# Optimization experiments

Hardware: AMD Instinct MI355X
Metric: run time of the kernel (lower is better)

## Reference

```python
import jax, jax.numpy as jnp
import numpy as np
from jax import lax
from jax.scipy.linalg import solve_triangular

# Newton-Schulz dynamic coefficients (6 iterations), from the source table
NS_COEFFS = [
    (3955/1024, -8306/1024, 5008/1024),
    (3735/1024, -6681/1024, 3463/1024),
    (3799/1024, -6499/1024, 3211/1024),
    (4019/1024, -6385/1024, 2906/1024),
    (2677/1024, -3029/1024, 1162/1024),
    (2172/1024, -1833/1024,  682/1024),
]

B, T, D, H, DK, DV = 4, 1024, 512, 8, 64, 64


def newton_schulz6(M):
    # M: (..., dv, dk), square (dv == dk) so no transpose branch is needed
    X = M / (jnp.linalg.norm(M, axis=(-2, -1), keepdims=True) + 1e-7)
    for a, b, c in NS_COEFFS:
        A = X @ jnp.swapaxes(X, -1, -2)
        Bm = b * A + c * (A @ A)
        X = a * X + Bm @ X
    return X


def setup_inputs() -> dict:
    key = jax.random.key(0)
    ks = jax.random.split(key, 9)
    s = 0.02  # weight init scale
    return {
        "x":  jax.random.normal(ks[0], (B, T, D), jnp.float32),
        "Wq": jax.random.normal(ks[1], (H * DK, D), jnp.float32) * s,
        "Wk": jax.random.normal(ks[2], (H * DK, D), jnp.float32) * s,
        "Wv": jax.random.normal(ks[3], (H * DV, D), jnp.float32) * s,
        "Ww": jax.random.normal(ks[4], (H * DK, D), jnp.float32) * s,
        "Wp": jax.random.normal(ks[5], (H * 2, D), jnp.float32) * s,
        "Wo": jax.random.normal(ks[6], (D, H * DV), jnp.float32) * s,
        "S0": jax.random.normal(ks[7], (H, DV, DK), jnp.float32),
        "M0": jnp.zeros((H, DV, DK), jnp.float32),
    }


def _forward(x, Wq, Wk, Wv, Ww, Wp, Wo, S0, M0):
    b, t, d = x.shape
    h, dv, dk = S0.shape

    def heads(W, e):  # (b,t,d) @ W.T -> (b,h,t,e)
        return (x @ W.T).reshape(b, t, h, e).transpose(0, 2, 1, 3)

    q = heads(Wq, dk)
    k = heads(Wk, dk)
    v = heads(Wv, dv)
    w = heads(Ww, dk)
    p = jax.nn.sigmoid((x @ Wp.T).reshape(b, t, h, 2).transpose(0, 2, 1, 3))
    eta, theta = p[..., 0], p[..., 1]  # (b,h,t)

    # delta-rule redundancy: u_t = v_t - softmax(w_t K_{<t}^T / sqrt(dk)) U_{<t}
    scores = jnp.einsum('bhtd,bhsd->bhts', w, k) / (dk ** 0.5)
    strict = jnp.tril(jnp.ones((t, t), bool), k=-1)  # s < t
    A = jax.nn.softmax(jnp.where(strict, scores, -1e30), axis=-1) * strict
    # (I + A) U = V  (unit lower-triangular solve == the sequential recurrence)
    U = solve_triangular(A, v, lower=True, unit_diagonal=True)  # (b,h,t,dv)

    # sequential state update over time (momentum + Newton-Schulz + S accumulation)
    tm = lambda a: jnp.moveaxis(a, 2, 0)  # time-major
    xs = (tm(U), tm(k), tm(q), jnp.moveaxis(eta, 2, 0), jnp.moveaxis(theta, 2, 0))

    @jax.checkpoint
    def step(carry, inp):
        S, M = carry
        u_t, k_t, q_t, eta_t, theta_t = inp  # (b,h,dv)/(b,h,dk)/(b,h)
        g = u_t[..., :, None] * k_t[..., None, :]        # (b,h,dv,dk)
        th = theta_t[..., None, None]
        M = th * M + (1.0 - th) * g
        Sp = newton_schulz6(M)
        S = S + eta_t[..., None, None] * Sp
        o = jnp.einsum('bhvk,bhk->bhv', S, q_t)
        return (S, M), o

    S_init = jnp.broadcast_to(S0, (b, h, dv, dk))
    M_init = jnp.broadcast_to(M0, (b, h, dv, dk))
    (_, _), O = lax.scan(step, (S_init, M_init), xs)  # O: (t,b,h,dv)

    o = O.transpose(1, 0, 2, 3).reshape(b, t, h * dv)
    return o @ Wo.T  # (b,t,d)


def reference(x, Wq, Wk, Wv, Ww, Wp, Wo, S0, M0):
    return _forward(x, Wq, Wk, Wv, Ww, Wp, Wo, S0, M0)
```

## Files before the change

### kernel.cpp

```cpp
#include <hip/hip_runtime.h>
#include <hip/hip_bf16.h>
#include <math.h>

#define Bn 4
#define Tn 1024
#define Dn 512
#define Hn 8
#define BHn 32
#define LDP 65
#define LDU 68
#define LH 72

typedef _Float16 f16x8 __attribute__((ext_vector_type(8)));
typedef _Float16 f16x4 __attribute__((ext_vector_type(4)));
typedef float    f32x4 __attribute__((ext_vector_type(4)));

__constant__ float NS_Ac[6] = {3955.0f/1024.0f, 3735.0f/1024.0f, 3799.0f/1024.0f,
                               4019.0f/1024.0f, 2677.0f/1024.0f, 2172.0f/1024.0f};
__constant__ float NS_Bc[6] = {-8306.0f/1024.0f, -6681.0f/1024.0f, -6499.0f/1024.0f,
                               -6385.0f/1024.0f, -3029.0f/1024.0f, -1833.0f/1024.0f};
__constant__ float NS_Cc[6] = {5008.0f/1024.0f, 3463.0f/1024.0f, 3211.0f/1024.0f,
                               2906.0f/1024.0f, 1162.0f/1024.0f,  682.0f/1024.0f};

__device__ __forceinline__ f32x4 mfma16(f16x4 a, f16x4 b, f32x4 c) {
  return __builtin_amdgcn_mfma_f32_16x16x16f16(a, b, c, 0, 0, 0);
}
__device__ __forceinline__ f32x4 mfma32(f16x8 a, f16x8 b, f32x4 c) {
  return __builtin_amdgcn_mfma_f32_16x16x32_f16(a, b, c, 0, 0, 0);
}

__device__ __forceinline__ f16x4 cvt4(f32x4 a) {
  f16x4 h;
  h[0] = (_Float16)a[0]; h[1] = (_Float16)a[1];
  h[2] = (_Float16)a[2]; h[3] = (_Float16)a[3];
  return h;
}

__device__ __forceinline__ f16x4 cvt4rtz(f32x4 a) {
  const auto lo = __builtin_amdgcn_cvt_pkrtz(a[0], a[1]);
  const auto hi = __builtin_amdgcn_cvt_pkrtz(a[2], a[3]);
  f16x4 h;
  h[0] = (_Float16)lo[0]; h[1] = (_Float16)lo[1];
  h[2] = (_Float16)hi[0]; h[3] = (_Float16)hi[1];
  return h;
}

__device__ __forceinline__ f16x8 pack8(f16x4 lo, f16x4 hi) {
  f16x8 o;
  o[0] = lo[0]; o[1] = lo[1]; o[2] = lo[2]; o[3] = lo[3];
  o[4] = hi[0]; o[5] = hi[1]; o[6] = hi[2]; o[7] = hi[3];
  return o;
}

__device__ __forceinline__ void set_half(f16x8& v, int h, f16x4 x) {
  if (h) { v[4] = x[0]; v[5] = x[1]; v[6] = x[2]; v[7] = x[3]; }
  else   { v[0] = x[0]; v[1] = x[1]; v[2] = x[2]; v[3] = x[3]; }
}

__device__ __forceinline__ f16x4 make_If(int r, int g) {
  const int dd = r - 4 * g;
  f16x4 If;
  If[0] = (dd == 0) ? (_Float16)1.f : (_Float16)0.f;
  If[1] = (dd == 1) ? (_Float16)1.f : (_Float16)0.f;
  If[2] = (dd == 2) ? (_Float16)1.f : (_Float16)0.f;
  If[3] = (dd == 3) ? (_Float16)1.f : (_Float16)0.f;
  return If;
}

__device__ __forceinline__ f16x8 ld_frag8(const _Float16* lds, int row, int c, int g) {
  const f16x4 lo = *reinterpret_cast<const f16x4*>(lds + row * LH + (2 * c) * 16 + 4 * g);
  const f16x4 hi = *reinterpret_cast<const f16x4*>(lds + row * LH + (2 * c + 1) * 16 + 4 * g);
  return pack8(lo, hi);
}



__device__ __forceinline__ void stage_tile_h(_Float16* __restrict__ dst,
                                             const float* __restrict__ src,
                                             int srcStride, int tid) {
#pragma unroll
  for (int i = 0; i < 4; ++i) {
    const int idx = tid + (i << 8);
    const int row = idx >> 4;
    const int c4  = (idx & 15) << 2;
    const float4 v = *reinterpret_cast<const float4*>(src + (size_t)row * srcStride + c4);
    f16x4 h;
    h[0] = (_Float16)v.x; h[1] = (_Float16)v.y; h[2] = (_Float16)v.z; h[3] = (_Float16)v.w;
    *reinterpret_cast<f16x4*>(dst + row * LH + c4) = h;
  }
}

__device__ __forceinline__ void stage_tile_u(float* __restrict__ dst,
                                             const float* __restrict__ src, int tid) {
#pragma unroll
  for (int i = 0; i < 4; ++i) {
    const int idx = tid + (i << 8);
    const int row = idx >> 4;
    const int c4  = (idx & 15) << 2;
    *reinterpret_cast<float4*>(dst + row * LDU + c4) =
        *reinterpret_cast<const float4*>(src + (size_t)row * 64 + c4);
  }
}

__device__ __forceinline__ void tri_solve_blocked(const float* __restrict__ Sc,
                                                  float* __restrict__ Ua, int tid) {
  const int dv = tid & 63;
  const int grp = tid >> 6;
#pragma unroll 1
  for (int db = 0; db < 4; ++db) {
    const int base = db * 16;
    if (grp == 0) {
#pragma unroll 1
      for (int rr = 1; rr < 16; ++rr) {
        float s = 0.f;
        for (int c = 0; c < rr; ++c)
          s = fmaf(Sc[(base + rr) * LDP + base + c], Ua[(base + c) * LDU + dv], s);
        Ua[(base + rr) * LDU + dv] -= s;
      }
    }
    __syncthreads();
    if (db < 3) {
      for (int r2 = base + 16 + grp; r2 < 64; r2 += 4) {
        float s = 0.f;
#pragma unroll
        for (int c = 0; c < 16; ++c)
          s = fmaf(Sc[r2 * LDP + base + c], Ua[(base + c) * LDU + dv], s);
        Ua[r2 * LDU + dv] -= s;
      }
    }
    __syncthreads();
  }
}


__global__ __launch_bounds__(256) void proj4_kernel(
    const float* __restrict__ x,
    const float* __restrict__ W0, const float* __restrict__ W1,
    const float* __restrict__ W2, const float* __restrict__ W3,
    float* __restrict__ o0, float* __restrict__ o1,
    float* __restrict__ o2, float* __restrict__ o3) {
  __shared__ __align__(16) _Float16 Af[64 * LH];
  __shared__ __align__(16) _Float16 Bf[64 * LH];
  const float* W; float* outp;
  switch (blockIdx.z) {
    case 0:  W = W0; outp = o0; break;
    case 1:  W = W1; outp = o1; break;
    case 2:  W = W2; outp = o2; break;
    default: W = W3; outp = o3; break;
  }
  const int tid = threadIdx.x;
  const int m0 = blockIdx.x * 64;
  const int n0 = blockIdx.y * 64;
  const int wid = tid >> 6, lane = tid & 63;
  const int r = lane & 15, g = lane >> 4;
  f32x4 acc[4] = {};
  for (int kt = 0; kt < Dn; kt += 64) {
    stage_tile_h(Af, x + (size_t)m0 * Dn + kt, Dn, tid);
    stage_tile_h(Bf, W + (size_t)n0 * Dn + kt, Dn, tid);
    __syncthreads();
    f16x8 a8[2];
#pragma unroll
    for (int c = 0; c < 2; ++c) a8[c] = ld_frag8(Af, 16 * wid + r, c, g);
#pragma unroll
    for (int jb = 0; jb < 4; ++jb) {
#pragma unroll
      for (int c = 0; c < 2; ++c)
        acc[jb] = mfma32(a8[c], ld_frag8(Bf, 16 * jb + r, c, g), acc[jb]);
    }
    __syncthreads();
  }
#pragma unroll
  for (int jb = 0; jb < 4; ++jb)
#pragma unroll
    for (int d = 0; d < 4; ++d) {
      const int m = m0 + 16 * wid + 4 * g + d;
      const int n = n0 + 16 * jb + r;
      const int b = m >> 10, t = m & 1023, h = n >> 6, e = n & 63;
      outp[(((size_t)(b * Hn + h)) * Tn + t) * 64 + e] = acc[jb][d];
    }
}

#define XSTR 516
__global__ __launch_bounds__(256) void wp_kernel(const float* __restrict__ x,
                                                 const float* __restrict__ Wp,
                                                 float* __restrict__ eta,
                                                 float* __restrict__ theta) {
  __shared__ float xs[16 * XSTR];
  __shared__ float wps[16 * XSTR];
  const int tid = threadIdx.x;
  const int r0 = blockIdx.x * 16;
#pragma unroll
  for (int i = 0; i < 8; ++i) {
    const int idx = tid + (i << 8);
    const int r = idx >> 7, c4 = (idx & 127) << 2;
    const float4 v = *reinterpret_cast<const float4*>(x + (size_t)(r0 + r) * Dn + c4);
    float* p = xs + r * XSTR + c4;
    p[0] = v.x; p[1] = v.y; p[2] = v.z; p[3] = v.w;
    const float4 wv = *reinterpret_cast<const float4*>(Wp + (size_t)r * Dn + c4);
    float* pw = wps + r * XSTR + c4;
    pw[0] = wv.x; pw[1] = wv.y; pw[2] = wv.z; pw[3] = wv.w;
  }
  __syncthreads();
  const int row = tid >> 4, col = tid & 15;
  float acc = 0.f;
#pragma unroll 8
  for (int k = 0; k < Dn; ++k) acc = fmaf(xs[row * XSTR + k], wps[col * XSTR + k], acc);
  const float sg = 1.f / (1.f + __expf(-acc));
  const int m = r0 + row, b = m >> 10, t = m & 1023, h = col >> 1;
  float* dst = (col & 1) ? theta : eta;
  dst[((size_t)(b * Hn + h)) * Tn + t] = sg;
}

__global__ __launch_bounds__(256) void rowstats_kernel(
    const float* __restrict__ wb, const float* __restrict__ kb,
    float* __restrict__ rowm, float* __restrict__ rowl) {
  __shared__ __align__(16) _Float16 Wh[64 * LH];
  __shared__ __align__(16) _Float16 Kh[64 * LH];
  const int tb = blockIdx.x, bh = blockIdx.y, t0 = tb * 64;
  const int tid = threadIdx.x, wid = tid >> 6, lane = tid & 63;
  const int r = lane & 15, g = lane >> 4;
  stage_tile_h(Wh, wb + ((size_t)bh * Tn + t0) * 64, 64, tid);
  float rm[4], rl[4];
#pragma unroll
  for (int d = 0; d < 4; ++d) { rm[d] = -INFINITY; rl[d] = 0.f; }
  __syncthreads();
  f16x8 wfr8[2];
#pragma unroll
  for (int c = 0; c < 2; ++c) wfr8[c] = ld_frag8(Wh, 16 * wid + r, c, g);
  for (int sb = 0; sb <= tb; ++sb) {
    __syncthreads();
    stage_tile_h(Kh, kb + ((size_t)bh * Tn + sb * 64) * 64, 64, tid);
    __syncthreads();
    float sv[4][4];
    float tmax[4] = {-INFINITY, -INFINITY, -INFINITY, -INFINITY};
#pragma unroll
    for (int jb = 0; jb < 4; ++jb) {
      f32x4 acc = {0.f, 0.f, 0.f, 0.f};
#pragma unroll
      for (int c = 0; c < 2; ++c)
        acc = mfma32(wfr8[c], ld_frag8(Kh, 16 * jb + r, c, g), acc);
      const int col = sb * 64 + 16 * jb + r;
#pragma unroll
      for (int d = 0; d < 4; ++d) {
        const int row = t0 + 16 * wid + 4 * g + d;
        const float s = (col < row) ? acc[d] * 0.125f : -INFINITY;
        sv[jb][d] = s;
        tmax[d] = fmaxf(tmax[d], s);
      }
    }
#pragma unroll
    for (int m = 1; m < 16; m <<= 1)
#pragma unroll
      for (int d = 0; d < 4; ++d) tmax[d] = fmaxf(tmax[d], __shfl_xor(tmax[d], m, 64));
#pragma unroll
    for (int d = 0; d < 4; ++d) {
      const float mnew  = fmaxf(rm[d], tmax[d]);
      const float msafe = (mnew == -INFINITY) ? 0.f : mnew;
      float s = __expf(sv[0][d] - msafe) + __expf(sv[1][d] - msafe) +
                __expf(sv[2][d] - msafe) + __expf(sv[3][d] - msafe);
#pragma unroll
      for (int m = 1; m < 16; m <<= 1) s += __shfl_xor(s, m, 64);
      const float scale = (rm[d] == -INFINITY) ? 0.f : __expf(rm[d] - msafe);
      rl[d] = rl[d] * scale + s;
      rm[d] = mnew;
    }
  }
  if (r == 0) {
#pragma unroll
    for (int d = 0; d < 4; ++d) {
      const int row = t0 + 16 * wid + 4 * g + d;
      rowm[(size_t)bh * Tn + row] = rm[d];
      rowl[(size_t)bh * Tn + row] = (rl[d] == 0.f) ? 1.f : rl[d];
    }
  }
}

__global__ __launch_bounds__(256) void copyU_kernel(const float* __restrict__ vb,
                                                    float* __restrict__ Ub) {
  const int gid = blockIdx.x * 256 + threadIdx.x;
  ((float4*)Ub)[gid] = ((const float4*)vb)[gid];
}

__global__ __launch_bounds__(256) void solve_diag0_kernel(
    const float* __restrict__ wb, const float* __restrict__ kb,
    const float* __restrict__ vb, const float* __restrict__ rowm,
    const float* __restrict__ rowl, float* __restrict__ Ub) {
  __shared__ __align__(16) _Float16 Wh[64 * LH];
  __shared__ __align__(16) _Float16 Kh[64 * LH];
  __shared__ float Sc[64 * LDP];
  __shared__ __align__(16) float Ua[64 * LDU];
  __shared__ float rmL[64], rlL[64];
  const int bh = blockIdx.x;
  const int tid = threadIdx.x, wid = tid >> 6, lane = tid & 63;
  const int r = lane & 15, g = lane >> 4;
  stage_tile_h(Wh, wb + (size_t)bh * Tn * 64, 64, tid);
  stage_tile_h(Kh, kb + (size_t)bh * Tn * 64, 64, tid);
  stage_tile_u(Ua, vb + (size_t)bh * Tn * 64, tid);
  if (tid < 64) { rmL[tid] = rowm[(size_t)bh * Tn + tid]; rlL[tid] = rowl[(size_t)bh * Tn + tid]; }
  __syncthreads();
  f16x4 wfr[4];
#pragma unroll
  for (int kc = 0; kc < 4; ++kc)
    wfr[kc] = *reinterpret_cast<const f16x4*>(Wh + (16 * wid + r) * LH + kc * 16 + 4 * g);
  float rmv[4], rlv[4];
#pragma unroll
  for (int d = 0; d < 4; ++d) {
    rmv[d] = rmL[16 * wid + 4 * g + d];
    rlv[d] = rlL[16 * wid + 4 * g + d];
  }
#pragma unroll
  for (int jb = 0; jb < 4; ++jb) {
    f32x4 acc = {0.f, 0.f, 0.f, 0.f};
#pragma unroll
    for (int kc = 0; kc < 4; ++kc)
      acc = mfma16(wfr[kc],
                   *reinterpret_cast<const f16x4*>(Kh + (16 * jb + r) * LH + kc * 16 + 4 * g),
                   acc);
#pragma unroll
    for (int d = 0; d < 4; ++d) {
      const int lr = 16 * wid + 4 * g + d, lc = 16 * jb + r;
      Sc[lr * LDP + lc] = (lc < lr) ? __expf(acc[d] * 0.125f - rmv[d]) / rlv[d] : 0.f;
    }
  }
  __syncthreads();
  tri_solve_blocked(Sc, Ua, tid);
#pragma unroll
  for (int i = 0; i < 4; ++i) {
    const int idx = tid + (i << 8);
    const int row = idx >> 4, c4 = (idx & 15) << 2;
    *reinterpret_cast<float4*>(Ub + ((size_t)bh * Tn + row) * 64 + c4) =
        *reinterpret_cast<const float4*>(Ua + row * LDU + c4);
  }
}

__global__ __launch_bounds__(256) void solve_step_kernel(
    const float* __restrict__ wb, const float* __restrict__ kb,
    const float* __restrict__ rowm, const float* __restrict__ rowl,
    float* __restrict__ Ub, int ib) {
  __shared__ __align__(16) _Float16 Wh[64 * LH];
  __shared__ __align__(16) _Float16 Kh[64 * LH];
  __shared__ __align__(16) _Float16 UTh[64 * LH];
  __shared__ float Sc[64 * LDP];
  __shared__ __align__(16) float Ua[64 * LDU];
  __shared__ float rmL[64], rlL[64];
  const int f = ib + 1 + blockIdx.x, bh = blockIdx.y;
  const int tid = threadIdx.x, wid = tid >> 6, lane = tid & 63;
  const int r = lane & 15, g = lane >> 4;
  stage_tile_h(Wh, wb + ((size_t)bh * Tn + f * 64) * 64, 64, tid);
  stage_tile_h(Kh, kb + ((size_t)bh * Tn + ib * 64) * 64, 64, tid);
  {
    const float* src = Ub + ((size_t)bh * Tn + ib * 64) * 64;
#pragma unroll
    for (int i2 = 0; i2 < 4; ++i2) {
      const int idx = tid + (i2 << 8);
      const int row = idx >> 4, c4 = (idx & 15) << 2;
      const float4 v = *reinterpret_cast<const float4*>(src + (size_t)row * 64 + c4);
      UTh[(c4 + 0) * LH + row] = (_Float16)v.x;
      UTh[(c4 + 1) * LH + row] = (_Float16)v.y;
      UTh[(c4 + 2) * LH + row] = (_Float16)v.z;
      UTh[(c4 + 3) * LH + row] = (_Float16)v.w;
    }
  }
  if (tid < 64) {
    rmL[tid] = rowm[(size_t)bh * Tn + f * 64 + tid];
    rlL[tid] = rowl[(size_t)bh * Tn + f * 64 + tid];
  }
  __syncthreads();
  f16x4 wfr[4];
#pragma unroll
  for (int kc = 0; kc < 4; ++kc)
    wfr[kc] = *reinterpret_cast<const f16x4*>(Wh + (16 * wid + r) * LH + kc * 16 + 4 * g);
  float rmv[4], rlv[4];
#pragma unroll
  for (int d = 0; d < 4; ++d) {
    rmv[d] = rmL[16 * wid + 4 * g + d];
    rlv[d] = rlL[16 * wid + 4 * g + d];
  }
  const f16x4 If = make_If(r, g);
  f16x4 Pfr[4];
#pragma unroll
  for (int jb = 0; jb < 4; ++jb) {
    f32x4 acc = {0.f, 0.f, 0.f, 0.f};
#pragma unroll
    for (int kc = 0; kc < 4; ++kc)
      acc = mfma16(wfr[kc],
                   *reinterpret_cast<const f16x4*>(Kh + (16 * jb + r) * LH + kc * 16 + 4 * g),
                   acc);
    f16x4 pf;
#pragma unroll
    for (int d = 0; d < 4; ++d)
      pf[d] = (_Float16)(-__expf(acc[d] * 0.125f - rmv[d]) / rlv[d]);
    Pfr[jb] = cvt4(mfma16(pf, If, (f32x4){0.f, 0.f, 0.f, 0.f}));
  }
  const float* uf = Ub + ((size_t)bh * Tn + f * 64) * 64;
  f32x4 acc2[4];
#pragma unroll
  for (int i = 0; i < 4; ++i) {
    const float4 v = *reinterpret_cast<const float4*>(uf + (size_t)(16 * wid + r) * 64 + 16 * i + 4 * g);
    acc2[i][0] = v.x; acc2[i][1] = v.y; acc2[i][2] = v.z; acc2[i][3] = v.w;
#pragma unroll
    for (int kc = 0; kc < 4; ++kc)
      acc2[i] = mfma16(*reinterpret_cast<const f16x4*>(UTh + (16 * i + r) * LH + kc * 16 + 4 * g),
                       Pfr[kc], acc2[i]);
  }
  if (f == ib + 1) {
    __syncthreads();
    stage_tile_h(Kh, kb + ((size_t)bh * Tn + f * 64) * 64, 64, tid);
#pragma unroll
    for (int i = 0; i < 4; ++i) {
      float4 v = {acc2[i][0], acc2[i][1], acc2[i][2], acc2[i][3]};
      *reinterpret_cast<float4*>(Ua + (16 * wid + r) * LDU + 16 * i + 4 * g) = v;
    }
    __syncthreads();
#pragma unroll
    for (int jb = 0; jb < 4; ++jb) {
      f32x4 acc = {0.f, 0.f, 0.f, 0.f};
#pragma unroll
      for (int kc = 0; kc < 4; ++kc)
        acc = mfma16(wfr[kc],
                     *reinterpret_cast<const f16x4*>(Kh + (16 * jb + r) * LH + kc * 16 + 4 * g),
                     acc);
#pragma unroll
      for (int d = 0; d < 4; ++d) {
        const int lr = 16 * wid + 4 * g + d, lc = 16 * jb + r;
        Sc[lr * LDP + lc] = (lc < lr) ? __expf(acc[d] * 0.125f - rmv[d]) / rlv[d] : 0.f;
      }
    }
    __syncthreads();
    tri_solve_blocked(Sc, Ua, tid);
#pragma unroll
    for (int i2 = 0; i2 < 4; ++i2) {
      const int idx = tid + (i2 << 8);
      const int row = idx >> 4, c4 = (idx & 15) << 2;
      *reinterpret_cast<float4*>(Ub + ((size_t)bh * Tn + f * 64 + row) * 64 + c4) =
          *reinterpret_cast<const float4*>(Ua + row * LDU + c4);
    }
  } else {
#pragma unroll
    for (int i = 0; i < 4; ++i) {
      float4 v = {acc2[i][0], acc2[i][1], acc2[i][2], acc2[i][3]};
      *reinterpret_cast<float4*>(Ub + ((size_t)bh * Tn + f * 64 + 16 * wid + r) * 64 + 16 * i + 4 * g) = v;
    }
  }
}

__global__ __launch_bounds__(256) void mscan_kernel(
    const float* __restrict__ Ub, const float* __restrict__ kb,
    const float* __restrict__ theta, float* __restrict__ Mcarry,
    _Float16* __restrict__ Mbuf, int t0, int Tc) {
  const int gid = blockIdx.x * 256 + threadIdx.x;
  const int bh = gid >> 12, p = gid & 4095;
  const int q = p >> 9, i = q >> 1, c = q & 1;
  const int l = (p >> 3) & 63, g = l >> 4, r = l & 15;
  const int s = p & 7, jhi = s >> 2, jlo = s & 3;
  const int dv = i * 16 + r;
  const int dk = c * 32 + jhi * 16 + g * 4 + jlo;
  float M = Mcarry[gid];
  const float* Urow = Ub + (size_t)bh * Tn * 64;
  const float* krow = kb + (size_t)bh * Tn * 64;
  const float* th   = theta + (size_t)bh * Tn;
  for (int tl = 0; tl < Tc; ++tl) {
    const int t = t0 + tl;
    const float thv = th[t];
    const float gg = Urow[(size_t)t * 64 + dv] * krow[(size_t)t * 64 + dk];
    M = thv * M + (1.f - thv) * gg;
    Mbuf[((size_t)bh * Tc + tl) * 4096 + p] = (_Float16)M;
  }
  Mcarry[gid] = M;
}

__global__ __launch_bounds__(256, 4) void ns_kernel(_Float16* __restrict__ Mbuf) {
  const int tid  = threadIdx.x;
  const int wid  = tid >> 6, lane = tid & 63;
  const int r    = lane & 15, g = lane >> 4;
  _Float16* src = Mbuf + ((size_t)blockIdx.x * 4 + wid) * 4096;

  f16x8 Xf8[4][2];
  float ss = 0.f;
#pragma unroll
  for (int i = 0; i < 4; ++i)
#pragma unroll
    for (int c = 0; c < 2; ++c) {
      const f16x8 h = *reinterpret_cast<const f16x8*>(src + (i * 2 + c) * 512 + lane * 8);
#pragma unroll
      for (int d = 0; d < 8; ++d) { const float f = (float)h[d]; ss += f * f; }
      Xf8[i][c] = h;
    }
#pragma unroll
  for (int off = 32; off > 0; off >>= 1) ss += __shfl_xor(ss, off, 64);
  const float inv = 1.f / (sqrtf(ss) + 1e-7f);
#pragma unroll
  for (int i = 0; i < 4; ++i)
#pragma unroll
    for (int c = 0; c < 2; ++c) {
      f32x4 lo, hi;
#pragma unroll
      for (int d = 0; d < 4; ++d) { lo[d] = (float)Xf8[i][c][d] * inv; hi[d] = (float)Xf8[i][c][d + 4] * inv; }
      Xf8[i][c] = pack8(cvt4rtz(lo), cvt4rtz(hi));
    }

  const f16x4 If = make_If(r, g);
  f16x4 zero4;
  zero4[0] = (_Float16)0.f; zero4[1] = (_Float16)0.f;
  zero4[2] = (_Float16)0.f; zero4[3] = (_Float16)0.f;
  const f16x8 I8[2] = {pack8(If, zero4), pack8(zero4, If)};
  float Iw[4];
  Iw[0] = (float)If[0]; Iw[1] = (float)If[1]; Iw[2] = (float)If[2]; Iw[3] = (float)If[3];

  f16x8 Ff8[4][2];
  f32x4 acc[4][4];

#pragma unroll 1
  for (int it = 0; it < 6; ++it) {
    const float ca = NS_Ac[it], cb = NS_Bc[it], cc = NS_Cc[it];
#pragma unroll
    for (int i = 0; i < 4; ++i)
#pragma unroll
      for (int j = i; j < 4; ++j) {
        f32x4 a = mfma32(Xf8[i][0], Xf8[j][0], (f32x4){0.f, 0.f, 0.f, 0.f});
        acc[i][j] = mfma32(Xf8[i][1], Xf8[j][1], a);
      }
#pragma unroll
    for (int i = 0; i < 4; ++i) {
      {
        const f16x4 t = cvt4rtz(mfma32(Xf8[i][i >> 1], I8[i & 1], (f32x4){0.f, 0.f, 0.f, 0.f}));
        set_half(Xf8[i][i >> 1], i & 1, t);
      }
#pragma unroll
      for (int j = i + 1; j < 4; ++j) {
        const f16x4 t1 = cvt4rtz(mfma32(Xf8[i][j >> 1], I8[j & 1], (f32x4){0.f, 0.f, 0.f, 0.f}));
        const f16x4 t2 = cvt4rtz(mfma32(Xf8[j][i >> 1], I8[i & 1], (f32x4){0.f, 0.f, 0.f, 0.f}));
        set_half(Xf8[j][i >> 1], i & 1, t1);
        set_half(Xf8[i][j >> 1], j & 1, t2);
      }
    }
#pragma unroll
    for (int i = 0; i < 4; ++i)
#pragma unroll
      for (int j = i; j < 4; ++j) set_half(Ff8[j][i >> 1], i & 1, cvt4rtz(acc[i][j]));
#pragma unroll
    for (int i = 0; i < 4; ++i)
#pragma unroll
      for (int j = i + 1; j < 4; ++j)
        set_half(Ff8[i][j >> 1], j & 1,
                 cvt4rtz(mfma32(Ff8[j][i >> 1], I8[i & 1], (f32x4){0.f, 0.f, 0.f, 0.f})));
    const float bc = cb / cc;
#pragma unroll
    for (int i = 0; i < 4; ++i)
#pragma unroll
      for (int j = i; j < 4; ++j) {
        f32x4 a = acc[i][j];
        a[0] *= bc; a[1] *= bc; a[2] *= bc; a[3] *= bc;
        a = mfma32(Ff8[i][0], Ff8[j][0], a);
        a = mfma32(Ff8[i][1], Ff8[j][1], a);
        a[0] *= cc; a[1] *= cc; a[2] *= cc; a[3] *= cc;
        acc[i][j] = a;
      }
#pragma unroll
    for (int i = 0; i < 4; ++i)
#pragma unroll
      for (int d = 0; d < 4; ++d) acc[i][i][d] = fmaf(ca, Iw[d], acc[i][i][d]);
#pragma unroll
    for (int i = 0; i < 4; ++i)
#pragma unroll
      for (int j = i; j < 4; ++j) set_half(Ff8[j][i >> 1], i & 1, cvt4rtz(acc[i][j]));
#pragma unroll
    for (int i = 0; i < 4; ++i)
#pragma unroll
      for (int j = i + 1; j < 4; ++j)
        set_half(Ff8[i][j >> 1], j & 1,
                 cvt4rtz(mfma32(Ff8[j][i >> 1], I8[i & 1], (f32x4){0.f, 0.f, 0.f, 0.f})));
#pragma unroll
    for (int i = 0; i < 4; ++i)
#pragma unroll
      for (int j = 0; j < 4; ++j) {
        f32x4 a = mfma32(Xf8[i][0], Ff8[j][0], (f32x4){0.f, 0.f, 0.f, 0.f});
        acc[i][j] = mfma32(Xf8[i][1], Ff8[j][1], a);
      }
    const bool last = (it == 5);
#pragma unroll
    for (int i = 0; i < 4; ++i)
#pragma unroll
      for (int j = 0; j < 4; ++j)
        set_half(Xf8[j][i >> 1], i & 1, last ? cvt4(acc[i][j]) : cvt4rtz(acc[i][j]));
  }

#pragma unroll
  for (int i = 0; i < 4; ++i)
#pragma unroll
    for (int c = 0; c < 2; ++c)
      *reinterpret_cast<f16x8*>(src + (i * 2 + c) * 512 + lane * 8) = Xf8[i][c];
}

__global__ __launch_bounds__(256) void gsum_kernel(
    const float* __restrict__ eta, const _Float16* __restrict__ Mbuf,
    float* __restrict__ Gbuf, int t0, int Tc) {
  const int j = blockIdx.x, bh = blockIdx.y, tid = threadIdx.x;
  const int nsub = Tc >> 4;
  float acc[16] = {};
#pragma unroll 1
  for (int i = 0; i < 16; ++i) {
    const int tl = j * 16 + i;
    const float ev = eta[(size_t)bh * Tn + t0 + tl];
    const _Float16* sp = Mbuf + ((size_t)bh * Tc + tl) * 4096;
    const f16x8 h0 = *reinterpret_cast<const f16x8*>(sp + tid * 8);
    const f16x8 h1 = *reinterpret_cast<const f16x8*>(sp + 2048 + tid * 8);
#pragma unroll
    for (int u = 0; u < 8; ++u) {
      acc[u]     += ev * (float)h0[u];
      acc[8 + u] += ev * (float)h1[u];
    }
  }
  float* g = Gbuf + ((size_t)bh * nsub + j) * 4096;
#pragma unroll
  for (int u = 0; u < 2; ++u) {
    float4 w0 = {acc[u*4], acc[u*4+1], acc[u*4+2], acc[u*4+3]};
    *reinterpret_cast<float4*>(g + tid * 8 + u * 4) = w0;
    float4 w1 = {acc[8+u*4], acc[8+u*4+1], acc[8+u*4+2], acc[8+u*4+3]};
    *reinterpret_cast<float4*>(g + 2048 + tid * 8 + u * 4) = w1;
  }
}

__global__ __launch_bounds__(256) void sbase_kernel(
    float* __restrict__ Scarry, const float* __restrict__ Gbuf,
    float* __restrict__ Sbase, int Tc) {
  const int gid = blockIdx.x * 256 + threadIdx.x;
  const int bh = gid >> 12, e = gid & 4095;
  const int nsub = Tc >> 4;
  float S = Scarry[gid];
  for (int j = 0; j < nsub; ++j) {
    const size_t idx = ((size_t)bh * nsub + j) * 4096 + e;
    Sbase[idx] = S;
    S += Gbuf[idx];
  }
  Scarry[gid] = S;
}

__global__ __launch_bounds__(256) void outv2_kernel(
    const float* __restrict__ eta, const float* __restrict__ qb,
    const float* __restrict__ Sbase, const _Float16* __restrict__ Mbuf,
    float* __restrict__ ob, int t0, int Tc) {
  const int j = blockIdx.x, bh = blockIdx.y, tid = threadIdx.x;
  const int nsub = Tc >> 4;
  const int ty = tid >> 4, tx = tid & 15;
  const int dv0 = ty * 4, dk0 = tx * 4;
  int off[4];
#pragma unroll
  for (int r2 = 0; r2 < 4; ++r2) {
    const int row = dv0 + r2;
    off[r2] = ((row >> 4) * 2 + (dk0 >> 5)) * 512 +
              (((dk0 & 15) >> 2) * 16 + (row & 15)) * 8 + ((dk0 >> 4) & 1) * 4;
  }
  float S[4][4];
  const float* sb = Sbase + ((size_t)bh * nsub + j) * 4096;
#pragma unroll
  for (int r2 = 0; r2 < 4; ++r2) {
    const float4 v = *reinterpret_cast<const float4*>(sb + off[r2]);
    S[r2][0] = v.x; S[r2][1] = v.y; S[r2][2] = v.z; S[r2][3] = v.w;
  }
#pragma unroll 1
  for (int i = 0; i < 16; ++i) {
    const int tl = j * 16 + i, t = t0 + tl;
    const float ev = eta[(size_t)bh * Tn + t];
    const float4 q4 = *reinterpret_cast<const float4*>(qb + ((size_t)bh * Tn + t) * 64 + dk0);
    const _Float16* sp = Mbuf + ((size_t)bh * Tc + tl) * 4096;
    float part[4];
#pragma unroll
    for (int r2 = 0; r2 < 4; ++r2) {
      const f16x4 h = *reinterpret_cast<const f16x4*>(sp + off[r2]);
      S[r2][0] += ev * (float)h[0];
      S[r2][1] += ev * (float)h[1];
      S[r2][2] += ev * (float)h[2];
      S[r2][3] += ev * (float)h[3];
      part[r2] = S[r2][0] * q4.x + S[r2][1] * q4.y + S[r2][2] * q4.z + S[r2][3] * q4.w;
    }
#pragma unroll
    for (int m = 1; m < 16; m <<= 1)
#pragma unroll
      for (int r2 = 0; r2 < 4; ++r2) part[r2] += __shfl_xor(part[r2], m, 64);
    if (tx == 0) {
      float4 o4 = {part[0], part[1], part[2], part[3]};
      *reinterpret_cast<float4*>(ob + ((size_t)bh * Tn + t) * 64 + dv0) = o4;
    }
  }
}

__global__ __launch_bounds__(256) void init_carry_kernel(
    const float* __restrict__ S0, const float* __restrict__ M0,
    float* __restrict__ Scarry, float* __restrict__ Mcarry) {
  const int gid = blockIdx.x * 256 + threadIdx.x;
  const int h = (gid >> 12) & 7, p = gid & 4095;
  const int q = p >> 9, i = q >> 1, c = q & 1;
  const int l = (p >> 3) & 63, g = l >> 4, r = l & 15;
  const int s = p & 7, jhi = s >> 2, jlo = s & 3;
  const int dv = i * 16 + r;
  const int dk = c * 32 + jhi * 16 + g * 4 + jlo;
  const int e = dv * 64 + dk;
  Scarry[gid] = S0[h * 4096 + e];
  Mcarry[gid] = M0[h * 4096 + e];
}

__global__ __launch_bounds__(256) void out_gemm_kernel(
    const float* __restrict__ ob, const float* __restrict__ Wo,
    float* __restrict__ out) {
  __shared__ __align__(16) _Float16 Af[64 * LH];
  __shared__ __align__(16) _Float16 Bf[64 * LH];
  const int tid = threadIdx.x;
  const int m0 = blockIdx.x * 64;
  const int n0 = blockIdx.y * 64;
  const int wid = tid >> 6, lane = tid & 63;
  const int r = lane & 15, g = lane >> 4;
  f32x4 acc[4] = {};
  for (int kt = 0; kt < Dn; kt += 64) {
    const int h = kt >> 6;
#pragma unroll
    for (int i = 0; i < 4; ++i) {
      const int idx = tid + (i << 8);
      const int row = idx >> 4, c4 = (idx & 15) << 2;
      const int m = m0 + row, b = m >> 10, t = m & 1023;
      const float4 v = *reinterpret_cast<const float4*>(
          ob + ((size_t)(b * Hn + h) * Tn + t) * 64 + c4);
      f16x4 hv;
      hv[0] = (_Float16)v.x; hv[1] = (_Float16)v.y; hv[2] = (_Float16)v.z; hv[3] = (_Float16)v.w;
      *reinterpret_cast<f16x4*>(Af + row * LH + c4) = hv;
    }
    stage_tile_h(Bf, Wo + (size_t)n0 * Dn + kt, Dn, tid);
    __syncthreads();
    f16x8 a8[2];
#pragma unroll
    for (int c = 0; c < 2; ++c) a8[c] = ld_frag8(Af, 16 * wid + r, c, g);
#pragma unroll
    for (int jb = 0; jb < 4; ++jb) {
#pragma unroll
      for (int c = 0; c < 2; ++c)
        acc[jb] = mfma32(a8[c], ld_frag8(Bf, 16 * jb + r, c, g), acc[jb]);
    }
    __syncthreads();
  }
#pragma unroll
  for (int jb = 0; jb < 4; ++jb)
#pragma unroll
    for (int d = 0; d < 4; ++d) {
      const int m = m0 + 16 * wid + 4 * g + d;
      const int n = n0 + 16 * jb + r;
      out[(size_t)m * Dn + n] = acc[jb][d];
    }
}


extern "C" void kernel_launch(void* const* d_in, const int* in_sizes, int n_in,
                              void* d_out, int out_size, void* d_ws, size_t ws_size,
                              hipStream_t stream) {
  (void)in_sizes; (void)n_in; (void)out_size;
  const float* x  = (const float*)d_in[0];
  const float* Wq = (const float*)d_in[1];
  const float* Wk = (const float*)d_in[2];
  const float* Wv = (const float*)d_in[3];
  const float* Ww = (const float*)d_in[4];
  const float* Wp = (const float*)d_in[5];
  const float* Wo = (const float*)d_in[6];
  const float* S0 = (const float*)d_in[7];
  const float* M0 = (const float*)d_in[8];
  float* out = (float*)d_out;
  float* ws  = (float*)d_ws;

  size_t off = 0;
  float* qb  = ws + off; off += (size_t)BHn * Tn * 64;
  float* kb  = ws + off; off += (size_t)BHn * Tn * 64;
  float* vb  = ws + off; off += (size_t)BHn * Tn * 64;
  float* wb  = ws + off; off += (size_t)BHn * Tn * 64;
  float* Ub  = ws + off; off += (size_t)BHn * Tn * 64;
  float* ob  = ws + off; off += (size_t)BHn * Tn * 64;
  float* eta   = ws + off; off += (size_t)BHn * Tn;
  float* theta = ws + off; off += (size_t)BHn * Tn;
  float* rowm  = ws + off; off += (size_t)BHn * Tn;
  float* rowl  = ws + off; off += (size_t)BHn * Tn;
  float* Mcarry = ws + off; off += (size_t)BHn * 4096;
  float* Scarry = ws + off; off += (size_t)BHn * 4096;

  const size_t avail0 = ws_size / sizeof(float) - off;
  int Tc = 512;
  while (Tc > 16 && (size_t)BHn * Tc * 2048 + 2 * (size_t)BHn * (Tc / 16) * 4096 > avail0)
    Tc >>= 1;
  const int nsub = Tc >> 4;

  float* Gbuf  = ws + off; off += (size_t)BHn * nsub * 4096;
  float* Sbase = ws + off; off += (size_t)BHn * nsub * 4096;
  _Float16* Mbuf = (_Float16*)(ws + off);

  hipLaunchKernelGGL(init_carry_kernel, dim3(512), dim3(256), 0, stream, S0, M0, Scarry, Mcarry);
  hipLaunchKernelGGL(proj4_kernel, dim3(64, 8, 4), dim3(256), 0, stream,
                     x, Wq, Wk, Wv, Ww, qb, kb, vb, wb);
  hipLaunchKernelGGL(wp_kernel, dim3(256), dim3(256), 0, stream, x, Wp, eta, theta);
  hipLaunchKernelGGL(rowstats_kernel, dim3(16, 32), dim3(256), 0, stream, wb, kb, rowm, rowl);
  hipLaunchKernelGGL(copyU_kernel, dim3(2048), dim3(256), 0, stream, vb, Ub);
  hipLaunchKernelGGL(solve_diag0_kernel, dim3(32), dim3(256), 0, stream,
                     wb, kb, vb, rowm, rowl, Ub);
  for (int ib = 0; ib < 15; ++ib) {
    hipLaunchKernelGGL(solve_step_kernel, dim3(15 - ib, 32), dim3(256), 0, stream,
                       wb, kb, rowm, rowl, Ub, ib);
  }

  for (int t0 = 0; t0 < Tn; t0 += Tc) {
    hipLaunchKernelGGL(mscan_kernel, dim3(512), dim3(256), 0, stream,
                       Ub, kb, theta, Mcarry, Mbuf, t0, Tc);
    hipLaunchKernelGGL(ns_kernel, dim3(BHn * Tc / 4), dim3(256), 0, stream, Mbuf);
    hipLaunchKernelGGL(gsum_kernel, dim3(nsub, BHn), dim3(256), 0, stream,
                       eta, Mbuf, Gbuf, t0, Tc);
    hipLaunchKernelGGL(sbase_kernel, dim3(512), dim3(256), 0, stream, Scarry, Gbuf, Sbase, Tc);
    hipLaunchKernelGGL(outv2_kernel, dim3(nsub, BHn), dim3(256), 0, stream,
                       eta, qb, Sbase, Mbuf, ob, t0, Tc);
  }

  hipLaunchKernelGGL(out_gemm_kernel, dim3(64, 8), dim3(256), 0, stream, ob, Wo, out);
}
```

Baseline: 1.307 ms.

## Parallelize momentum scan over time chunks with three-phase chunked scan

Replaces the sequential per-element momentum scan, which walks all Tc timesteps in one thread across only 512 blocks, with a three-phase chunked linear scan. Phase A computes each 32-step chunk's local contribution in parallel. Phase B propagates chunk start states using precomputed theta products. Phase C recomputes each chunk from its start state and writes fp16 M with vectorized stores. It also raises ns_kernel's occupancy hint to 8 blocks per SM. The cost is reading U/k twice and extra scratch traffic, with Gbuf and Sbase reused as Rbuf and Mstart.

Result: slower. 3.498 ms (+167.6%).

```diff
diff --git a/kernel.cpp b/kernel.cpp
--- a/kernel.cpp
+++ b/kernel.cpp
@@ -10,6 +10,7 @@
 #define LDP 65
 #define LDU 68
 #define LH 72
+#define TS 32
 
 typedef _Float16 f16x8 __attribute__((ext_vector_type(8)));
 typedef _Float16 f16x4 __attribute__((ext_vector_type(4)));
@@ -444,32 +445,120 @@
   }
 }
 
-__global__ __launch_bounds__(256) void mscan_kernel(
+__global__ __launch_bounds__(256) void thetaprod_kernel(
+    const float* __restrict__ theta, float* __restrict__ TP) {
+  const int idx = blockIdx.x * 256 + threadIdx.x;
+  if (idx >= BHn * (Tn / TS)) return;
+  const int bh = idx / (Tn / TS), jg = idx % (Tn / TS);
+  const float* th = theta + (size_t)bh * Tn + jg * TS;
+  float p = 1.f;
+#pragma unroll
+  for (int s = 0; s < TS; ++s) p *= th[s];
+  TP[idx] = p;
+}
+
+__global__ __launch_bounds__(256) void mscanA_kernel(
     const float* __restrict__ Ub, const float* __restrict__ kb,
-    const float* __restrict__ theta, float* __restrict__ Mcarry,
-    _Float16* __restrict__ Mbuf, int t0, int Tc) {
+    const float* __restrict__ theta, float* __restrict__ Rbuf,
+    int t0, int Tc) {
+  const int j = blockIdx.x, bh = blockIdx.y, tid = threadIdx.x;
+  const int nsub = Tc / TS;
+  const int chunk = tid >> 5, l0 = (2 * tid) & 63;
+  const int i = chunk >> 1, c = chunk & 1, g = l0 >> 4;
+  const int dv0 = i * 16 + (l0 & 15);
+  const int kbase = c * 32 + g * 4;
+  const int tb = t0 + j * TS;
+  const float* Urow = Ub + ((size_t)bh * Tn + tb) * 64;
+  const float* krow = kb + ((size_t)bh * Tn + tb) * 64;
+  const float* th   = theta + (size_t)bh * Tn + tb;
+  float M[2][8] = {};
+#pragma unroll 2
+  for (int st = 0; st < TS; ++st) {
+    const float thv = th[st], om = 1.f - thv;
+    const float2 uv = *reinterpret_cast<const float2*>(Urow + (size_t)st * 64 + dv0);
+    const float4 k0 = *reinterpret_cast<const float4*>(krow + (size_t)st * 64 + kbase);
+    const float4 k1 = *reinterpret_cast<const float4*>(krow + (size_t)st * 64 + kbase + 16);
+    const float kv[8] = {k0.x, k0.y, k0.z, k0.w, k1.x, k1.y, k1.z, k1.w};
+    const float ou[2] = {om * uv.x, om * uv.y};
+#pragma unroll
+    for (int gq = 0; gq < 2; ++gq)
+#pragma unroll
+      for (int s = 0; s < 8; ++s)
+        M[gq][s] = fmaf(thv, M[gq][s], ou[gq] * kv[s]);
+  }
+  float* rp = Rbuf + ((size_t)bh * nsub + j) * 4096 + tid * 16;
+#pragma unroll
+  for (int gq = 0; gq < 2; ++gq)
+#pragma unroll
+    for (int h = 0; h < 2; ++h) {
+      float4 v = {M[gq][h*4], M[gq][h*4+1], M[gq][h*4+2], M[gq][h*4+3]};
+      *reinterpret_cast<float4*>(rp + gq * 8 + h * 4) = v;
+    }
+}
+
+__global__ __launch_bounds__(256) void mscanB_kernel(
+    float* __restrict__ Mcarry, const float* __restrict__ Rbuf,
+    const float* __restrict__ TP, float* __restrict__ Mstart,
+    int t0, int Tc) {
   const int gid = blockIdx.x * 256 + threadIdx.x;
   const int bh = gid >> 12, p = gid & 4095;
-  const int q = p >> 9, i = q >> 1, c = q & 1;
-  const int l = (p >> 3) & 63, g = l >> 4, r = l & 15;
-  const int s = p & 7, jhi = s >> 2, jlo = s & 3;
-  const int dv = i * 16 + r;
-  const int dk = c * 32 + jhi * 16 + g * 4 + jlo;
+  const int nsub = Tc / TS;
+  const int jg0 = t0 / TS;
   float M = Mcarry[gid];
-  const float* Urow = Ub + (size_t)bh * Tn * 64;
-  const float* krow = kb + (size_t)bh * Tn * 64;
-  const float* th   = theta + (size_t)bh * Tn;
-  for (int tl = 0; tl < Tc; ++tl) {
-    const int t = t0 + tl;
-    const float thv = th[t];
-    const float gg = Urow[(size_t)t * 64 + dv] * krow[(size_t)t * 64 + dk];
-    M = thv * M + (1.f - thv) * gg;
-    Mbuf[((size_t)bh * Tc + tl) * 4096 + p] = (_Float16)M;
+  for (int j = 0; j < nsub; ++j) {
+    const size_t idx = ((size_t)bh * nsub + j) * 4096 + p;
+    Mstart[idx] = M;
+    M = TP[bh * (Tn / TS) + jg0 + j] * M + Rbuf[idx];
   }
   Mcarry[gid] = M;
 }
 
-__global__ __launch_bounds__(256, 4) void ns_kernel(_Float16* __restrict__ Mbuf) {
+__global__ __launch_bounds__(256) void mscanC_kernel(
+    const float* __restrict__ Ub, const float* __restrict__ kb,
+    const float* __restrict__ theta, const float* __restrict__ Mstart,
+    _Float16* __restrict__ Mbuf, int t0, int Tc) {
+  const int j = blockIdx.x, bh = blockIdx.y, tid = threadIdx.x;
+  const int nsub = Tc / TS;
+  const int chunk = tid >> 5, l0 = (2 * tid) & 63;
+  const int i = chunk >> 1, c = chunk & 1, g = l0 >> 4;
+  const int dv0 = i * 16 + (l0 & 15);
+  const int kbase = c * 32 + g * 4;
+  const int tb = t0 + j * TS;
+  const float* Urow = Ub + ((size_t)bh * Tn + tb) * 64;
+  const float* krow = kb + ((size_t)bh * Tn + tb) * 64;
+  const float* th   = theta + (size_t)bh * Tn + tb;
+  float M[2][8];
+  const float* mp = Mstart + ((size_t)bh * nsub + j) * 4096 + tid * 16;
+#pragma unroll
+  for (int gq = 0; gq < 2; ++gq)
+#pragma unroll
+    for (int h = 0; h < 2; ++h) {
+      const float4 v = *reinterpret_cast<const float4*>(mp + gq * 8 + h * 4);
+      M[gq][h*4] = v.x; M[gq][h*4+1] = v.y; M[gq][h*4+2] = v.z; M[gq][h*4+3] = v.w;
+    }
+#pragma unroll 2
+  for (int st = 0; st < TS; ++st) {
+    const float thv = th[st], om = 1.f - thv;
+    const float2 uv = *reinterpret_cast<const float2*>(Urow + (size_t)st * 64 + dv0);
+    const float4 k0 = *reinterpret_cast<const float4*>(krow + (size_t)st * 64 + kbase);
+    const float4 k1 = *reinterpret_cast<const float4*>(krow + (size_t)st * 64 + kbase + 16);
+    const float kv[8] = {k0.x, k0.y, k0.z, k0.w, k1.x, k1.y, k1.z, k1.w};
+    const float ou[2] = {om * uv.x, om * uv.y};
+    _Float16* dst = Mbuf + ((size_t)bh * Tc + j * TS + st) * 4096 + tid * 16;
+#pragma unroll
+    for (int gq = 0; gq < 2; ++gq) {
+      f16x8 hh;
+#pragma unroll
+      for (int s = 0; s < 8; ++s) {
+        M[gq][s] = fmaf(thv, M[gq][s], ou[gq] * kv[s]);
+        hh[s] = (_Float16)M[gq][s];
+      }
+      *reinterpret_cast<f16x8*>(dst + gq * 8) = hh;
+    }
+  }
+}
+
+__global__ __launch_bounds__(256, 8) void ns_kernel(_Float16* __restrict__ Mbuf) {
   const int tid  = threadIdx.x;
   const int wid  = tid >> 6, lane = tid & 63;
   const int r    = lane & 15, g = lane >> 4;
@@ -777,21 +866,27 @@
   float* rowl  = ws + off; off += (size_t)BHn * Tn;
   float* Mcarry = ws + off; off += (size_t)BHn * 4096;
   float* Scarry = ws + off; off += (size_t)BHn * 4096;
+  float* TP     = ws + off; off += (size_t)BHn * (Tn / TS);
 
   const size_t avail0 = ws_size / sizeof(float) - off;
   int Tc = 512;
-  while (Tc > 16 && (size_t)BHn * Tc * 2048 + 2 * (size_t)BHn * (Tc / 16) * 4096 > avail0)
+  while (Tc > TS && (size_t)BHn * Tc * 2048 + 2 * (size_t)BHn * (Tc / 16) * 4096 > avail0)
     Tc >>= 1;
   const int nsub = Tc >> 4;
+  const int nsubT = Tc / TS;
 
   float* Gbuf  = ws + off; off += (size_t)BHn * nsub * 4096;
   float* Sbase = ws + off; off += (size_t)BHn * nsub * 4096;
   _Float16* Mbuf = (_Float16*)(ws + off);
+  float* Rbuf   = Gbuf;
+  float* Mstart = Sbase;
 
   hipLaunchKernelGGL(init_carry_kernel, dim3(512), dim3(256), 0, stream, S0, M0, Scarry, Mcarry);
   hipLaunchKernelGGL(proj4_kernel, dim3(64, 8, 4), dim3(256), 0, stream,
                      x, Wq, Wk, Wv, Ww, qb, kb, vb, wb);
   hipLaunchKernelGGL(wp_kernel, dim3(256), dim3(256), 0, stream, x, Wp, eta, theta);
+  hipLaunchKernelGGL(thetaprod_kernel, dim3((BHn * (Tn / TS) + 255) / 256), dim3(256), 0, stream,
+                     theta, TP);
   hipLaunchKernelGGL(rowstats_kernel, dim3(16, 32), dim3(256), 0, stream, wb, kb, rowm, rowl);
   hipLaunchKernelGGL(copyU_kernel, dim3(2048), dim3(256), 0, stream, vb, Ub);
   hipLaunchKernelGGL(solve_diag0_kernel, dim3(32), dim3(256), 0, stream,
@@ -802,8 +897,12 @@
   }
 
   for (int t0 = 0; t0 < Tn; t0 += Tc) {
-    hipLaunchKernelGGL(mscan_kernel, dim3(512), dim3(256), 0, stream,
-                       Ub, kb, theta, Mcarry, Mbuf, t0, Tc);
+    hipLaunchKernelGGL(mscanA_kernel, dim3(nsubT, BHn), dim3(256), 0, stream,
+                       Ub, kb, theta, Rbuf, t0, Tc);
+    hipLaunchKernelGGL(mscanB_kernel, dim3(512), dim3(256), 0, stream,
+                       Mcarry, Rbuf, TP, Mstart, t0, Tc);
+    hipLaunchKernelGGL(mscanC_kernel, dim3(nsubT, BHn), dim3(256), 0, stream,
+                       Ub, kb, theta, Mstart, Mbuf, t0, Tc);
     hipLaunchKernelGGL(ns_kernel, dim3(BHn * Tc / 4), dim3(256), 0, stream, Mbuf);
     hipLaunchKernelGGL(gsum_kernel, dim3(nsub, BHn), dim3(256), 0, stream,
                        eta, Mbuf, Gbuf, t0, Tc);
```
